# Kernel optimization log

Measured on AMD Instinct MI355X. Metric: run time of the kernel, lower is better.

Reference implementation:

```python
import jax, jax.numpy as jnp
import numpy as np

DIM = 1024
EPS = 1e-12  # torch F.normalize eps


def setup_inputs() -> dict:
    key = jax.random.key(0)
    k1, k2, k3 = jax.random.split(key, 3)
    b, n, d = 2, 4096, DIM
    x = jax.random.normal(k1, (b, n, d), dtype=jnp.float32)
    # nn.Linear(dim, 3*dim, bias=False): weight shape [3*dim, dim]
    w_qkva = jax.random.normal(k2, (3 * d, d), dtype=jnp.float32) * (1.0 / np.sqrt(d))
    gamma = jnp.ones((d,), dtype=jnp.float32)  # RMSNorm gamma (init ones)
    return {"x": x, "gamma": gamma, "w_qkva": w_qkva}


def _rmsnorm(x, gamma):
    # lucidrains RMSNorm: F.normalize(x, dim=-1) * sqrt(dim) * gamma
    norm = jnp.sqrt(jnp.sum(x * x, axis=-1, keepdims=True))
    scale = jnp.asarray(np.sqrt(x.shape[-1]), x.dtype)
    return x / jnp.maximum(norm, EPS) * scale * gamma


def reference(x, gamma, w_qkva):
    d = x.shape[-1]
    xn = _rmsnorm(x, gamma)
    qkva = jnp.einsum('bnd,ed->bne', xn, w_qkva)  # [b, n, 3d]
    q, kv, a = qkva[..., :d], qkva[..., d:2 * d], qkva[..., 2 * d:]
    a = jax.nn.sigmoid(a)

    def binary_operator(e_i, e_j):
        a_i, kv_i = e_i
        a_j, kv_j = e_j
        return a_j * a_i, a_j * kv_i + kv_j

    # per-channel scalar linear recurrence: kv_t = a_t * kv_{t-1} + kv_t
    _, kv_scan = jax.lax.associative_scan(binary_operator, (a, kv), axis=1)
    return q * kv_scan  # [b, n, d]
```

## Files before the change

kernel.cpp:

```cpp
#include <hip/hip_runtime.h>
#include <cstdint>
#include <cstddef>

#define DIMD 1024
#define BB 2
#define NN 4096
#define MM (BB*NN)
#define EE (3*DIMD)
#define KK DIMD

typedef __attribute__((ext_vector_type(8))) short short8;
typedef __attribute__((ext_vector_type(4))) float f32x4;

__device__ __forceinline__ unsigned short f2bf(float f) {
  unsigned int u = __float_as_uint(f);
  u += 0x7FFF + ((u >> 16) & 1);
  return (unsigned short)(u >> 16);
}

#define GLOAD_LDS16(gptr, lptr) \
  __builtin_amdgcn_global_load_lds((const __attribute__((address_space(1))) void*)(gptr), \
                                   (__attribute__((address_space(3))) void*)(lptr), 16, 0, 0)

__global__ void cast_w_kernel(const float* __restrict__ w, unsigned short* __restrict__ wb) {
  int i = blockIdx.x * blockDim.x + threadIdx.x;
  const float4* w4 = (const float4*)w;
  float4 v = w4[i];
  unsigned int lo = (unsigned int)f2bf(v.x) | ((unsigned int)f2bf(v.y) << 16);
  unsigned int hi = (unsigned int)f2bf(v.z) | ((unsigned int)f2bf(v.w) << 16);
  ((uint2*)wb)[i] = make_uint2(lo, hi);
}

__global__ void rmsnorm_kernel(const float* __restrict__ x, const float* __restrict__ gamma,
                               unsigned short* __restrict__ xn) {
  int row = blockIdx.x;
  int tid = threadIdx.x;
  const float4* x4 = (const float4*)(x + (size_t)row * DIMD);
  float4 v = x4[tid];
  float ss = v.x*v.x + v.y*v.y + v.z*v.z + v.w*v.w;
  #pragma unroll
  for (int m = 32; m >= 1; m >>= 1) ss += __shfl_xor(ss, m);
  __shared__ float red[4];
  if ((tid & 63) == 0) red[tid >> 6] = ss;
  __syncthreads();
  float tot = red[0] + red[1] + red[2] + red[3];
  float scale = 32.0f / fmaxf(sqrtf(tot), 1e-12f);
  const float4* g4 = (const float4*)gamma;
  float4 g = g4[tid];
  float a0 = v.x*scale*g.x, a1 = v.y*scale*g.y, a2 = v.z*scale*g.z, a3 = v.w*scale*g.w;
  unsigned int lo = (unsigned int)f2bf(a0) | ((unsigned int)f2bf(a1) << 16);
  unsigned int hi = (unsigned int)f2bf(a2) | ((unsigned int)f2bf(a3) << 16);
  ((uint2*)(xn + (size_t)row * DIMD))[tid] = make_uint2(lo, hi);
}

#define BM 128
#define BN 128
#define BK 64
#define NT (KK/BK)

__global__ __launch_bounds__(256) void gemm_kernel(const unsigned short* __restrict__ A,
                                                   const unsigned short* __restrict__ Bw,
                                                   float* __restrict__ q_pl,
                                                   float* __restrict__ kv_pl,
                                                   float* __restrict__ a_pl) {
  __shared__ unsigned short Al[2][BM][BK];
  __shared__ unsigned short Bl[2][BN][BK];
  int tid = threadIdx.x;
  int l = tid & 63;
  int w = tid >> 6;
  int wr = w >> 1, wc = w & 1;
  int m0 = blockIdx.y * BM;
  int n0 = blockIdx.x * BN;
  int lrow = l & 15, lk = l >> 4;

  int srow = w * 32 + (l >> 3);
  int scol = (((l & 7) ^ (l >> 3)) * 8);
  const unsigned short* Ag = A  + (size_t)(m0 + srow) * KK + scol;
  const unsigned short* Bg = Bw + (size_t)(n0 + srow) * KK + scol;

  f32x4 acc[4][4];
  #pragma unroll
  for (int i = 0; i < 4; i++)
    #pragma unroll
    for (int j = 0; j < 4; j++) acc[i][j] = (f32x4)(0.f);

  #pragma unroll
  for (int t = 0; t < 4; t++) {
    GLOAD_LDS16(Ag + (size_t)(t*8) * KK, &Al[0][w*32 + t*8][0]);
    GLOAD_LDS16(Bg + (size_t)(t*8) * KK, &Bl[0][w*32 + t*8][0]);
  }
  __syncthreads();

  int cur = 0;
  for (int kt = 0; kt < NT; ++kt) {
    if (kt + 1 < NT) {
      int nk = (kt + 1) * BK;
      #pragma unroll
      for (int t = 0; t < 4; t++) {
        GLOAD_LDS16(Ag + (size_t)(t*8) * KK + nk, &Al[cur ^ 1][w*32 + t*8][0]);
        GLOAD_LDS16(Bg + (size_t)(t*8) * KK + nk, &Bl[cur ^ 1][w*32 + t*8][0]);
      }
    }
    #pragma unroll
    for (int s = 0; s < 2; s++) {
      short8 af[4], bf[4];
      #pragma unroll
      for (int i = 0; i < 4; i++) {
        int r = wr*64 + i*16 + lrow;
        af[i] = *(const short8*)&Al[cur][r][((s*4 + lk) ^ (r & 7)) * 8];
      }
      #pragma unroll
      for (int j = 0; j < 4; j++) {
        int r = wc*64 + j*16 + lrow;
        bf[j] = *(const short8*)&Bl[cur][r][((s*4 + lk) ^ (r & 7)) * 8];
      }
      #pragma unroll
      for (int i = 0; i < 4; i++)
        #pragma unroll
        for (int j = 0; j < 4; j++)
          acc[i][j] = __builtin_amdgcn_mfma_f32_16x16x32_bf16(af[i], bf[j], acc[i][j], 0, 0, 0);
    }
    if (kt + 1 < NT) {
      __syncthreads();
      cur ^= 1;
    }
  }

  int plane = n0 >> 10;
  float* P = (plane == 0) ? q_pl : ((plane == 1) ? kv_pl : a_pl);
  bool isg = (plane == 2);
  int pn0 = n0 & 1023;
  #pragma unroll
  for (int i = 0; i < 4; i++) {
    int rowb = m0 + wr*64 + i*16 + lk*4;
    #pragma unroll
    for (int j = 0; j < 4; j++) {
      int pcol = pn0 + wc*64 + j*16 + lrow;
      f32x4 v = acc[i][j];
      #pragma unroll
      for (int r = 0; r < 4; r++) {
        float val = v[r];
        if (isg) val = 1.0f / (1.0f + __expf(-val));
        P[(size_t)(rowb + r)*DIMD + pcol] = val;
      }
    }
  }
}

#define CHUNK 32
#define NCH (NN / CHUNK)

__global__ void scan1_kernel(const float* __restrict__ kv_pl, const float* __restrict__ a_pl,
                             float* __restrict__ Aagg, float* __restrict__ Kagg) {
  int d = threadIdx.x * 4;
  int c = blockIdx.x;
  int b = blockIdx.y;
  size_t base = ((size_t)(b*NN + c*CHUNK)) * DIMD + d;
  const float* pa = a_pl + base;
  const float* pk = kv_pl + base;
  float4 Aa = make_float4(1.f,1.f,1.f,1.f);
  float4 Kv = make_float4(0.f,0.f,0.f,0.f);
  for (int i0 = 0; i0 < CHUNK; i0 += 4) {
    float4 av[4], kvv[4];
    #pragma unroll
    for (int u = 0; u < 4; u++) av[u]  = *(const float4*)&pa[(size_t)(i0+u)*DIMD];
    #pragma unroll
    for (int u = 0; u < 4; u++) kvv[u] = *(const float4*)&pk[(size_t)(i0+u)*DIMD];
    #pragma unroll
    for (int u = 0; u < 4; u++) {
      Kv.x = fmaf(av[u].x, Kv.x, kvv[u].x); Aa.x *= av[u].x;
      Kv.y = fmaf(av[u].y, Kv.y, kvv[u].y); Aa.y *= av[u].y;
      Kv.z = fmaf(av[u].z, Kv.z, kvv[u].z); Aa.z *= av[u].z;
      Kv.w = fmaf(av[u].w, Kv.w, kvv[u].w); Aa.w *= av[u].w;
    }
  }
  size_t idx = (size_t)(b*NCH + c)*DIMD + d;
  *(float4*)&Aagg[idx] = Aa;
  *(float4*)&Kagg[idx] = Kv;
}

__global__ void scan2_kernel(const float* __restrict__ Aagg, const float* __restrict__ Kagg,
                             float* __restrict__ carry) {
  int t = blockIdx.x * 256 + threadIdx.x;
  int b = t >> 10, d = t & (DIMD - 1);
  float cy = 0.f;
  for (int c0 = 0; c0 < NCH; c0 += 8) {
    float Av[8], Kv[8];
    #pragma unroll
    for (int u = 0; u < 8; u++) {
      size_t idx = (size_t)(b*NCH + c0 + u)*DIMD + d;
      Av[u] = Aagg[idx]; Kv[u] = Kagg[idx];
    }
    #pragma unroll
    for (int u = 0; u < 8; u++) {
      carry[(size_t)(b*NCH + c0 + u)*DIMD + d] = cy;
      cy = fmaf(Av[u], cy, Kv[u]);
    }
  }
}

__global__ void scan3_kernel(const float* __restrict__ q_pl, const float* __restrict__ kv_pl,
                             const float* __restrict__ a_pl, const float* __restrict__ carry,
                             float* __restrict__ out) {
  int d = threadIdx.x * 4;
  int c = blockIdx.x;
  int b = blockIdx.y;
  size_t base = ((size_t)(b*NN + c*CHUNK)) * DIMD + d;
  const float* pa = a_pl + base;
  const float* pk = kv_pl + base;
  const float* pq = q_pl + base;
  float* o = out + base;
  float4 Kv = *(const float4*)&carry[(size_t)(b*NCH + c)*DIMD + d];
  for (int i0 = 0; i0 < CHUNK; i0 += 4) {
    float4 av[4], kvv[4], qv[4];
    #pragma unroll
    for (int u = 0; u < 4; u++) av[u]  = *(const float4*)&pa[(size_t)(i0+u)*DIMD];
    #pragma unroll
    for (int u = 0; u < 4; u++) kvv[u] = *(const float4*)&pk[(size_t)(i0+u)*DIMD];
    #pragma unroll
    for (int u = 0; u < 4; u++) qv[u]  = *(const float4*)&pq[(size_t)(i0+u)*DIMD];
    #pragma unroll
    for (int u = 0; u < 4; u++) {
      float4 r;
      Kv.x = fmaf(av[u].x, Kv.x, kvv[u].x); r.x = qv[u].x * Kv.x;
      Kv.y = fmaf(av[u].y, Kv.y, kvv[u].y); r.y = qv[u].y * Kv.y;
      Kv.z = fmaf(av[u].z, Kv.z, kvv[u].z); r.z = qv[u].z * Kv.z;
      Kv.w = fmaf(av[u].w, Kv.w, kvv[u].w); r.w = qv[u].w * Kv.w;
      *(float4*)&o[(size_t)(i0+u)*DIMD] = r;
    }
  }
}

extern "C" void kernel_launch(void* const* d_in, const int* in_sizes, int n_in,
                              void* d_out, int out_size, void* d_ws, size_t ws_size,
                              hipStream_t stream) {
  const float* x     = (const float*)d_in[0];
  const float* gamma = (const float*)d_in[1];
  const float* wq    = (const float*)d_in[2];
  float* out = (float*)d_out;
  char* ws = (char*)d_ws;

  unsigned short* Wb = (unsigned short*)ws;
  unsigned short* Xn = (unsigned short*)(ws + 6291456);
  float* q_pl        = (float*)(ws + 23068672);
  float* kv_pl       = (float*)(ws + 56623104);
  float* a_pl        = (float*)(ws + 90177536);
  float* Aagg        = (float*)(ws + 123731968);
  float* Kagg        = (float*)(ws + 124780544);
  float* carry       = (float*)(ws + 125829120);

  cast_w_kernel<<<(EE*KK)/(256*4), 256, 0, stream>>>(wq, Wb);
  rmsnorm_kernel<<<MM, 256, 0, stream>>>(x, gamma, Xn);
  gemm_kernel<<<dim3(EE/BN, MM/BM), 256, 0, stream>>>(Xn, Wb, q_pl, kv_pl, a_pl);
  scan1_kernel<<<dim3(NCH, BB), 256, 0, stream>>>(kv_pl, a_pl, Aagg, Kagg);
  scan2_kernel<<<dim3((BB*DIMD)/256), 256, 0, stream>>>(Aagg, Kagg, carry);
  scan3_kernel<<<dim3(NCH, BB), 256, 0, stream>>>(q_pl, kv_pl, a_pl, carry, out);
}
```

Before: 201.5 us.

## Store kv and gate planes as bf16 and swizzle GEMM workgroup order

The GEMM epilogue now writes the kv and sigmoid-gate planes as bf16 instead of fp32. The two scan kernels read them as ushort4 and widen them back to float, which halves the intermediate traffic for those planes. Workgroup indices are also remapped with an XCD-style swizzle, so consecutive blocks are spread across the chip's XCDs and L2 locality may improve. Rounding kv and the gate to bf16 adds error to the recurrence, and that error can compound over long scans.

After: 198.8 us. Within noise of the previous version (-1.3%).

```diff
diff --git a/kernel.cpp b/kernel.cpp
--- a/kernel.cpp
+++ b/kernel.cpp
@@ -16,6 +16,9 @@
   unsigned int u = __float_as_uint(f);
   u += 0x7FFF + ((u >> 16) & 1);
   return (unsigned short)(u >> 16);
+}
+__device__ __forceinline__ float bf2f(unsigned short h) {
+  return __uint_as_float((unsigned int)h << 16);
 }
 
 #define GLOAD_LDS16(gptr, lptr) \
@@ -57,20 +60,25 @@
 #define BN 128
 #define BK 64
 #define NT (KK/BK)
+#define NWGX 24
+#define NWGY 64
 
 __global__ __launch_bounds__(256) void gemm_kernel(const unsigned short* __restrict__ A,
                                                    const unsigned short* __restrict__ Bw,
                                                    float* __restrict__ q_pl,
-                                                   float* __restrict__ kv_pl,
-                                                   float* __restrict__ a_pl) {
+                                                   unsigned short* __restrict__ kv_pl,
+                                                   unsigned short* __restrict__ a_pl) {
   __shared__ unsigned short Al[2][BM][BK];
   __shared__ unsigned short Bl[2][BN][BK];
   int tid = threadIdx.x;
   int l = tid & 63;
   int w = tid >> 6;
   int wr = w >> 1, wc = w & 1;
-  int m0 = blockIdx.y * BM;
-  int n0 = blockIdx.x * BN;
+
+  int lin = blockIdx.y * NWGX + blockIdx.x;
+  int swz = (lin & 7) * (NWGX * NWGY / 8) + (lin >> 3);
+  int n0 = (swz % NWGX) * BN;
+  int m0 = (swz / NWGX) * BM;
   int lrow = l & 15, lk = l >> 4;
 
   int srow = w * 32 + (l >> 3);
@@ -127,8 +135,6 @@
   }
 
   int plane = n0 >> 10;
-  float* P = (plane == 0) ? q_pl : ((plane == 1) ? kv_pl : a_pl);
-  bool isg = (plane == 2);
   int pn0 = n0 & 1023;
   #pragma unroll
   for (int i = 0; i < 4; i++) {
@@ -140,8 +146,14 @@
       #pragma unroll
       for (int r = 0; r < 4; r++) {
         float val = v[r];
-        if (isg) val = 1.0f / (1.0f + __expf(-val));
-        P[(size_t)(rowb + r)*DIMD + pcol] = val;
+        size_t idx = (size_t)(rowb + r)*DIMD + pcol;
+        if (plane == 0) {
+          q_pl[idx] = val;
+        } else if (plane == 1) {
+          kv_pl[idx] = f2bf(val);
+        } else {
+          a_pl[idx] = f2bf(1.0f / (1.0f + __expf(-val)));
+        }
       }
     }
   }
@@ -150,28 +162,30 @@
 #define CHUNK 32
 #define NCH (NN / CHUNK)
 
-__global__ void scan1_kernel(const float* __restrict__ kv_pl, const float* __restrict__ a_pl,
+__global__ void scan1_kernel(const unsigned short* __restrict__ kv_pl,
+                             const unsigned short* __restrict__ a_pl,
                              float* __restrict__ Aagg, float* __restrict__ Kagg) {
   int d = threadIdx.x * 4;
   int c = blockIdx.x;
   int b = blockIdx.y;
   size_t base = ((size_t)(b*NN + c*CHUNK)) * DIMD + d;
-  const float* pa = a_pl + base;
-  const float* pk = kv_pl + base;
+  const unsigned short* pa = a_pl + base;
+  const unsigned short* pk = kv_pl + base;
   float4 Aa = make_float4(1.f,1.f,1.f,1.f);
   float4 Kv = make_float4(0.f,0.f,0.f,0.f);
   for (int i0 = 0; i0 < CHUNK; i0 += 4) {
-    float4 av[4], kvv[4];
-    #pragma unroll
-    for (int u = 0; u < 4; u++) av[u]  = *(const float4*)&pa[(size_t)(i0+u)*DIMD];
-    #pragma unroll
-    for (int u = 0; u < 4; u++) kvv[u] = *(const float4*)&pk[(size_t)(i0+u)*DIMD];
+    ushort4 au[4], ku[4];
+    #pragma unroll
+    for (int u = 0; u < 4; u++) au[u] = *(const ushort4*)&pa[(size_t)(i0+u)*DIMD];
+    #pragma unroll
+    for (int u = 0; u < 4; u++) ku[u] = *(const ushort4*)&pk[(size_t)(i0+u)*DIMD];
     #pragma unroll
     for (int u = 0; u < 4; u++) {
-      Kv.x = fmaf(av[u].x, Kv.x, kvv[u].x); Aa.x *= av[u].x;
-      Kv.y = fmaf(av[u].y, Kv.y, kvv[u].y); Aa.y *= av[u].y;
-      Kv.z = fmaf(av[u].z, Kv.z, kvv[u].z); Aa.z *= av[u].z;
-      Kv.w = fmaf(av[u].w, Kv.w, kvv[u].w); Aa.w *= av[u].w;
+      float ax = bf2f(au[u].x), ay = bf2f(au[u].y), az = bf2f(au[u].z), aw = bf2f(au[u].w);
+      Kv.x = fmaf(ax, Kv.x, bf2f(ku[u].x)); Aa.x *= ax;
+      Kv.y = fmaf(ay, Kv.y, bf2f(ku[u].y)); Aa.y *= ay;
+      Kv.z = fmaf(az, Kv.z, bf2f(ku[u].z)); Aa.z *= az;
+      Kv.w = fmaf(aw, Kv.w, bf2f(ku[u].w)); Aa.w *= aw;
     }
   }
   size_t idx = (size_t)(b*NCH + c)*DIMD + d;
@@ -199,33 +213,37 @@
   }
 }
 
-__global__ void scan3_kernel(const float* __restrict__ q_pl, const float* __restrict__ kv_pl,
-                             const float* __restrict__ a_pl, const float* __restrict__ carry,
+__global__ void scan3_kernel(const float* __restrict__ q_pl,
+                             const unsigned short* __restrict__ kv_pl,
+                             const unsigned short* __restrict__ a_pl,
+                             const float* __restrict__ carry,
                              float* __restrict__ out) {
   int d = threadIdx.x * 4;
   int c = blockIdx.x;
   int b = blockIdx.y;
   size_t base = ((size_t)(b*NN + c*CHUNK)) * DIMD + d;
-  const float* pa = a_pl + base;
-  const float* pk = kv_pl + base;
+  const unsigned short* pa = a_pl + base;
+  const unsigned short* pk = kv_pl + base;
   const float* pq = q_pl + base;
   float* o = out + base;
   float4 Kv = *(const float4*)&carry[(size_t)(b*NCH + c)*DIMD + d];
   for (int i0 = 0; i0 < CHUNK; i0 += 4) {
-    float4 av[4], kvv[4], qv[4];
-    #pragma unroll
-    for (int u = 0; u < 4; u++) av[u]  = *(const float4*)&pa[(size_t)(i0+u)*DIMD];
-    #pragma unroll
-    for (int u = 0; u < 4; u++) kvv[u] = *(const float4*)&pk[(size_t)(i0+u)*DIMD];
-    #pragma unroll
-    for (int u = 0; u < 4; u++) qv[u]  = *(const float4*)&pq[(size_t)(i0+u)*DIMD];
+    ushort4 au[4], ku[4];
+    float4 qv[4];
+    #pragma unroll
+    for (int u = 0; u < 4; u++) au[u] = *(const ushort4*)&pa[(size_t)(i0+u)*DIMD];
+    #pragma unroll
+    for (int u = 0; u < 4; u++) ku[u] = *(const ushort4*)&pk[(size_t)(i0+u)*DIMD];
+    #pragma unroll
+    for (int u = 0; u < 4; u++) qv[u] = *(const float4*)&pq[(size_t)(i0+u)*DIMD];
     #pragma unroll
     for (int u = 0; u < 4; u++) {
+      float ax = bf2f(au[u].x), ay = bf2f(au[u].y), az = bf2f(au[u].z), aw = bf2f(au[u].w);
       float4 r;
-      Kv.x = fmaf(av[u].x, Kv.x, kvv[u].x); r.x = qv[u].x * Kv.x;
-      Kv.y = fmaf(av[u].y, Kv.y, kvv[u].y); r.y = qv[u].y * Kv.y;
-      Kv.z = fmaf(av[u].z, Kv.z, kvv[u].z); r.z = qv[u].z * Kv.z;
-      Kv.w = fmaf(av[u].w, Kv.w, kvv[u].w); r.w = qv[u].w * Kv.w;
+      Kv.x = fmaf(ax, Kv.x, bf2f(ku[u].x)); r.x = qv[u].x * Kv.x;
+      Kv.y = fmaf(ay, Kv.y, bf2f(ku[u].y)); r.y = qv[u].y * Kv.y;
+      Kv.z = fmaf(az, Kv.z, bf2f(ku[u].z)); r.z = qv[u].z * Kv.z;
+      Kv.w = fmaf(aw, Kv.w, bf2f(ku[u].w)); r.w = qv[u].w * Kv.w;
       *(float4*)&o[(size_t)(i0+u)*DIMD] = r;
     }
   }
@@ -240,18 +258,18 @@
   float* out = (float*)d_out;
   char* ws = (char*)d_ws;
 
-  unsigned short* Wb = (unsigned short*)ws;
-  unsigned short* Xn = (unsigned short*)(ws + 6291456);
-  float* q_pl        = (float*)(ws + 23068672);
-  float* kv_pl       = (float*)(ws + 56623104);
-  float* a_pl        = (float*)(ws + 90177536);
-  float* Aagg        = (float*)(ws + 123731968);
-  float* Kagg        = (float*)(ws + 124780544);
-  float* carry       = (float*)(ws + 125829120);
+  unsigned short* Wb   = (unsigned short*)ws;
+  unsigned short* Xn   = (unsigned short*)(ws + 6291456);
+  float* q_pl          = (float*)(ws + 23068672);
+  unsigned short* kv_pl= (unsigned short*)(ws + 56623104);
+  unsigned short* a_pl = (unsigned short*)(ws + 73400320);
+  float* Aagg          = (float*)(ws + 90177536);
+  float* Kagg          = (float*)(ws + 91226112);
+  float* carry         = (float*)(ws + 92274688);
 
   cast_w_kernel<<<(EE*KK)/(256*4), 256, 0, stream>>>(wq, Wb);
   rmsnorm_kernel<<<MM, 256, 0, stream>>>(x, gamma, Xn);
-  gemm_kernel<<<dim3(EE/BN, MM/BM), 256, 0, stream>>>(Xn, Wb, q_pl, kv_pl, a_pl);
+  gemm_kernel<<<dim3(NWGX, NWGY), 256, 0, stream>>>(Xn, Wb, q_pl, kv_pl, a_pl);
   scan1_kernel<<<dim3(NCH, BB), 256, 0, stream>>>(kv_pl, a_pl, Aagg, Kagg);
   scan2_kernel<<<dim3((BB*DIMD)/256), 256, 0, stream>>>(Aagg, Kagg, carry);
   scan3_kernel<<<dim3(NCH, BB), 256, 0, stream>>>(q_pl, kv_pl, a_pl, carry, out);
```
